# Performance work log

Hardware: AMD Instinct MI355X
Metric: run time of the kernel (lower is better)

Reference implementation:

```python
import jax, jax.numpy as jnp
import numpy as np

B, T, D = 16, 8192, 512
NHEAD, NKV = 8, 2
HD = D // NHEAD            # 64
KV_DIM = NKV * HD          # 128
N_REP = NHEAD // NKV       # 4
SCALE = 1.0 / np.sqrt(HD)


def setup_inputs() -> dict:
    key = jax.random.key(0)
    ks = jax.random.split(key, 8)
    w = 0.02
    return {
        "query": jax.random.normal(ks[0], (B, D), dtype=jnp.float32),
        "enc": jax.random.normal(ks[1], (B, T, D), dtype=jnp.float32),
        "Wq": jax.random.normal(ks[2], (D, D), dtype=jnp.float32) * w,
        "Wk": jax.random.normal(ks[3], (D, KV_DIM), dtype=jnp.float32) * w,
        "Wv": jax.random.normal(ks[4], (D, KV_DIM), dtype=jnp.float32) * w,
        "W1": jax.random.normal(ks[5], (2 * D, 4 * D), dtype=jnp.float32) * w,
        "W2": jax.random.normal(ks[6], (4 * D, D), dtype=jnp.float32) * w,
    }


def reference(query, enc, Wq, Wk, Wv, W1, W2):
    # Q projection: single decoder step -> [B, H, HD]
    q = (query @ Wq).reshape(B, NHEAD, HD)
    # K/V projections (GQA): [B, T, NKV, HD] -> [B, NKV, T, HD]
    k = (enc @ Wk).reshape(B, T, NKV, HD).transpose(0, 2, 1, 3)
    v = (enc @ Wv).reshape(B, T, NKV, HD).transpose(0, 2, 1, 3)
    # repeat KV heads to match query heads: [B, H, T, HD]
    k = jnp.repeat(k, N_REP, axis=1)
    v = jnp.repeat(v, N_REP, axis=1)
    # scaled dot-product attention, Tq == 1
    scores = jnp.einsum("bhd,bhtd->bht", q, k) * SCALE        # [B, H, T]
    attn = jax.nn.softmax(scores, axis=-1)
    context = jnp.einsum("bht,bhtd->bhd", attn, v).reshape(B, D)
    # combine context with query through SwiGLU-style MLP (Linear-SiLU-Linear)
    h = jnp.concatenate([context, query], axis=-1)            # [B, 2D]
    out = jax.nn.silu(h @ W1) @ W2                            # [B, D]
    return out
```

## Files before the change

### kernel.cpp

```cpp
#include <hip/hip_runtime.h>
#include <hip/hip_bf16.h>
#include <cstdint>
#include <cstddef>

#define BB 16
#define TT 8192
#define DD 512
#define NHEAD 8
#define NKV 2
#define HD 64
#define KVD 128
#define SCALE 0.125f

#define RB 64
#define NCHUNK (TT / RB)
#define BK 32
#define NSTEP (DD / BK)

typedef __attribute__((ext_vector_type(8))) short bf16x8;
typedef __attribute__((ext_vector_type(4))) float f32x4;

#define WS_Q      0
#define WS_WBT    8192
#define WS_OPART  73728
#define WS_ML     1122304
#define WS_H      1155072
#define WS_APART  1171456
#define WS_M2     1728512

__device__ __forceinline__ ushort f2bf(float f) {
    uint u = __builtin_bit_cast(uint, f);
    u += 0x7fffu + ((u >> 16) & 1u);
    return (ushort)(u >> 16);
}
__device__ __forceinline__ uint cvtpk(float a, float b) {
    uint r;
    asm("v_cvt_pk_bf16_f32 %0, %1, %2" : "=v"(r) : "v"(a), "v"(b));
    return r;
}
__device__ __forceinline__ float bf1(ushort s) {
    return __builtin_bit_cast(float, (uint)s << 16);
}
__device__ __forceinline__ float bflo(uint u) {
    return __builtin_bit_cast(float, u << 16);
}
__device__ __forceinline__ float bfhi(uint u) {
    return __builtin_bit_cast(float, u & 0xffff0000u);
}
__device__ __forceinline__ void gload_lds16(const void* g, void* l) {
    __builtin_amdgcn_global_load_lds((const __attribute__((address_space(1))) uint32_t*)g,
                                     (__attribute__((address_space(3))) uint32_t*)l, 16, 0, 0);
}

__global__ __launch_bounds__(256) void k_prep(const float* __restrict__ Wk,
                                              const float* __restrict__ Wv,
                                              const float* __restrict__ query,
                                              const float* __restrict__ Wq,
                                              ushort* __restrict__ wbt4,
                                              float* __restrict__ wsq) {
    const int t = threadIdx.x;
    if (blockIdx.x < 64) {
        const int G0 = blockIdx.x * 2048 + t * 8;
        const int s = G0 >> 13, r = G0 & 8191;
        const int fid = r >> 9, lane = (r >> 3) & 63;
        const int col = (fid >> 2) * 64 + (fid & 3) * 16 + (lane & 15);
        const int kbase = s * 32 + (lane >> 4) * 8;
        const float* W = (col < KVD) ? (Wk + col) : (Wv + (col - KVD));
#pragma unroll
        for (int e = 0; e < 8; ++e)
            wbt4[G0 + e] = f2bf(W[(size_t)(kbase + e) * KVD]);
    } else {
        __shared__ float qrow[DD];
        const int x = blockIdx.x - 64;
        const int b = x >> 1, half = x & 1;
        qrow[t] = query[b * DD + t];
        qrow[t + 256] = query[b * DD + t + 256];
        __syncthreads();
        const int col = half * 256 + t;
        float a0 = 0.f;
#pragma unroll 8
        for (int d = 0; d < DD; ++d) a0 = fmaf(qrow[d], Wq[(size_t)d * DD + col], a0);
        wsq[b * DD + col] = a0;
    }
}

__global__ __launch_bounds__(256) void k_attn(const float* __restrict__ enc,
                                              const ushort* __restrict__ wbt4,
                                              const float* __restrict__ wsq,
                                              float* __restrict__ o_part,
                                              float* __restrict__ ml) {
    __shared__ __align__(16) char smem[40960];
    __shared__ float sc[NHEAD * RB];
    __shared__ float qs[DD];

    const int tid = threadIdx.x;
    const int chunk = blockIdx.x, b = blockIdx.y;
    const int lane = tid & 63, w = tid >> 6;

    qs[tid] = wsq[b * DD + tid] * SCALE;
    qs[tid + 256] = wsq[b * DD + tid + 256] * SCALE;

    char* const A0 = smem;
    char* const A1 = smem + 4096;
    char* const B0 = smem + 8192;
    char* const B1 = smem + 24576;
    ushort* const kvl = (ushort*)smem;

    const float* encb = enc + ((size_t)b * TT + (size_t)chunk * RB) * DD;

    const int srow = (tid >> 6) * 16 + (tid & 15);
    const int skb = ((tid >> 4) & 3) * 8;

    f32x4 acc[4][4];
#pragma unroll
    for (int i = 0; i < 4; ++i)
#pragma unroll
        for (int j = 0; j < 4; ++j) acc[i][j] = (f32x4){0.f, 0.f, 0.f, 0.f};

    float4 e0, e1;

#define LOAD_ENC(ss)                                                                 \
    {                                                                                \
        const float* p_ = encb + (size_t)srow * DD + (ss) * BK + skb;                \
        e0 = *(const float4*)p_;                                                     \
        e1 = *(const float4*)(p_ + 4);                                               \
    }
#define WRITE_A(Abuf)                                                                \
    {                                                                                \
        uint4 u_;                                                                    \
        u_.x = cvtpk(e0.x, e0.y);                                                    \
        u_.y = cvtpk(e0.z, e0.w);                                                    \
        u_.z = cvtpk(e1.x, e1.y);                                                    \
        u_.w = cvtpk(e1.z, e1.w);                                                    \
        *(uint4*)((Abuf) + tid * 16) = u_;                                           \
    }
#define GLL_B(Bbuf, ss)                                                              \
    {                                                                                \
        _Pragma("unroll") for (int j = 0; j < 4; ++j)                                \
            gload_lds16(wbt4 + (size_t)(ss) * 8192 + (j * 256 + tid) * 8,            \
                        (Bbuf) + j * 4096 + w * 1024);                               \
    }

    LOAD_ENC(0);
    GLL_B(B0, 0);
    WRITE_A(A0);
    LOAD_ENC(1);

    for (int s = 0; s < NSTEP; ++s) {
        const int cur = s & 1;
        char* const Ac = cur ? A1 : A0;
        char* const Bc = cur ? B1 : B0;
        char* const An = cur ? A0 : A1;
        char* const Bn = cur ? B0 : B1;
        __syncthreads();
        if (s + 1 < NSTEP) {
            GLL_B(Bn, s + 1);
            WRITE_A(An);
            if (s + 2 < NSTEP) LOAD_ENC(s + 2);
        }
        bf16x8 bfr[4], af[4];
#pragma unroll
        for (int nt = 0; nt < 4; ++nt)
            bfr[nt] = *(const bf16x8*)(Bc + ((w * 4 + nt) * 64 + lane) * 16);
#pragma unroll
        for (int rt = 0; rt < 4; ++rt)
            af[rt] = *(const bf16x8*)(Ac + (rt * 64 + lane) * 16);
#pragma unroll
        for (int rt = 0; rt < 4; ++rt)
#pragma unroll
            for (int nt = 0; nt < 4; ++nt)
                acc[rt][nt] = __builtin_amdgcn_mfma_f32_16x16x32_bf16(
                    af[rt], bfr[nt], acc[rt][nt], 0, 0, 0);
    }

    const int h0 = w * 2;
    const int kvh = h0 >> 2;

    __syncthreads();
#pragma unroll
    for (int rt = 0; rt < 4; ++rt)
#pragma unroll
        for (int nt = 0; nt < 4; ++nt) {
            const int col = w * 64 + nt * 16 + (lane & 15);
#pragma unroll
            for (int j = 0; j < 4; ++j) {
                const int row = rt * 16 + (lane >> 4) * 4 + j;
                kvl[row * 258 + col] = f2bf(acc[rt][nt][j]);
            }
        }
    __syncthreads();

    {
        const float* qh0 = qs + h0 * HD;
        const float* qh1 = qs + (h0 + 1) * HD;
        const uint* kr = (const uint*)(kvl + lane * 258 + kvh * HD);
        float s0 = 0.f, s1 = 0.f;
#pragma unroll
        for (int d2 = 0; d2 < 32; ++d2) {
            const uint u = kr[d2];
            const float klo = bflo(u), khi = bfhi(u);
            s0 = fmaf(klo, qh0[2 * d2], s0);
            s0 = fmaf(khi, qh0[2 * d2 + 1], s0);
            s1 = fmaf(klo, qh1[2 * d2], s1);
            s1 = fmaf(khi, qh1[2 * d2 + 1], s1);
        }
        sc[h0 * RB + lane] = s0;
        sc[(h0 + 1) * RB + lane] = s1;
    }
    __syncthreads();

    {
        float mx0 = -1e30f, mx1 = -1e30f;
#pragma unroll 8
        for (int r = 0; r < RB; ++r) {
            mx0 = fmaxf(mx0, sc[h0 * RB + r]);
            mx1 = fmaxf(mx1, sc[(h0 + 1) * RB + r]);
        }
        float l0 = 0.f, l1 = 0.f, o0 = 0.f, o1 = 0.f;
        const ushort* vcol = kvl + KVD + kvh * HD + lane;
#pragma unroll 4
        for (int r = 0; r < RB; ++r) {
            const float vv = bf1(vcol[r * 258]);
            const float p0 = __expf(sc[h0 * RB + r] - mx0);
            const float p1 = __expf(sc[(h0 + 1) * RB + r] - mx1);
            l0 += p0; o0 = fmaf(p0, vv, o0);
            l1 += p1; o1 = fmaf(p1, vv, o1);
        }
        const size_t base0 = ((size_t)b * NCHUNK + chunk) * NHEAD + h0;
        o_part[base0 * HD + lane] = o0;
        o_part[(base0 + 1) * HD + lane] = o1;
        if (lane == 0) {
            ml[base0 * 2] = mx0; ml[base0 * 2 + 1] = l0;
            ml[(base0 + 1) * 2] = mx1; ml[(base0 + 1) * 2 + 1] = l1;
        }
    }
#undef LOAD_ENC
#undef WRITE_A
#undef GLL_B
}

__global__ __launch_bounds__(512) void k_reduce(const float* __restrict__ o_part,
                                                const float* __restrict__ ml,
                                                const float* __restrict__ query,
                                                float* __restrict__ hvec) {
    __shared__ float sEl[NHEAD][NCHUNK];
    const int b = blockIdx.x, t = threadIdx.x;
    const int h = t >> 6, lane = t & 63;

    const size_t ma_i = (((size_t)b * NCHUNK + lane) * NHEAD + h) * 2;
    const size_t mb_i = (((size_t)b * NCHUNK + lane + 64) * NHEAD + h) * 2;
    const float ma = ml[ma_i], la = ml[ma_i + 1];
    const float mb = ml[mb_i], lb = ml[mb_i + 1];
    float M = fmaxf(ma, mb);
#pragma unroll
    for (int off = 32; off >= 1; off >>= 1) M = fmaxf(M, __shfl_xor(M, off));
    const float ea = __expf(ma - M), eb = __expf(mb - M);
    float L = la * ea + lb * eb;
#pragma unroll
    for (int off = 32; off >= 1; off >>= 1) L += __shfl_xor(L, off);
    sEl[h][lane] = ea;
    sEl[h][lane + 64] = eb;
    __syncthreads();

    float O = 0.f;
#pragma unroll 4
    for (int i = 0; i < NCHUNK; ++i) {
        const size_t base = ((size_t)b * NCHUNK + i) * NHEAD + h;
        O = fmaf(o_part[base * HD + lane], sEl[h][i], O);
    }
    hvec[b * 1024 + h * HD + lane] = O / L;
    hvec[b * 1024 + 512 + t] = query[b * DD + t];
}

__global__ __launch_bounds__(256) void k_mlp1(const float* __restrict__ hvec,
                                              const float* __restrict__ W1,
                                              float* __restrict__ apart) {
    const int jb = blockIdx.x, ib = blockIdx.y;
    const int j = jb * 256 + threadIdx.x;
    float acc[BB];
#pragma unroll
    for (int b = 0; b < BB; ++b) acc[b] = 0.f;
    for (int i0 = ib * 64; i0 < ib * 64 + 64; i0 += 4) {
        const float w0 = W1[(size_t)(i0 + 0) * 2048 + j];
        const float w1 = W1[(size_t)(i0 + 1) * 2048 + j];
        const float w2 = W1[(size_t)(i0 + 2) * 2048 + j];
        const float w3 = W1[(size_t)(i0 + 3) * 2048 + j];
#pragma unroll
        for (int b = 0; b < BB; ++b) {
            const float* hb = hvec + b * 1024 + i0;
            acc[b] = fmaf(hb[0], w0, acc[b]);
            acc[b] = fmaf(hb[1], w1, acc[b]);
            acc[b] = fmaf(hb[2], w2, acc[b]);
            acc[b] = fmaf(hb[3], w3, acc[b]);
        }
    }
#pragma unroll
    for (int b = 0; b < BB; ++b)
        apart[((size_t)ib * BB + b) * 2048 + j] = acc[b];
}

__global__ __launch_bounds__(256) void k_mlp2(const float* __restrict__ apart,
                                              const float* __restrict__ W2,
                                              float* __restrict__ m2part) {
    __shared__ float actl[256];
    const int jb = blockIdx.x, b = blockIdx.y, ib = blockIdx.z;
    const int t = threadIdx.x;
    {
        const int jglob = ib * 256 + t;
        float s = 0.f;
#pragma unroll
        for (int p = 0; p < 16; ++p) s += apart[((size_t)p * BB + b) * 2048 + jglob];
        actl[t] = s / (1.f + __expf(-s));
    }
    __syncthreads();
    const int d = jb * 256 + t;
    float acc = 0.f;
    for (int j0 = 0; j0 < 256; j0 += 4) {
        const int jg = ib * 256 + j0;
        acc = fmaf(actl[j0 + 0], W2[(size_t)(jg + 0) * 512 + d], acc);
        acc = fmaf(actl[j0 + 1], W2[(size_t)(jg + 1) * 512 + d], acc);
        acc = fmaf(actl[j0 + 2], W2[(size_t)(jg + 2) * 512 + d], acc);
        acc = fmaf(actl[j0 + 3], W2[(size_t)(jg + 3) * 512 + d], acc);
    }
    m2part[((size_t)ib * BB + b) * 512 + d] = acc;
}

__global__ __launch_bounds__(512) void k_out(const float* __restrict__ m2part,
                                             float* __restrict__ out) {
    const int b = blockIdx.x, t = threadIdx.x;
    float s = 0.f;
#pragma unroll
    for (int ib = 0; ib < 8; ++ib) s += m2part[((size_t)ib * BB + b) * 512 + t];
    out[b * DD + t] = s;
}

extern "C" void kernel_launch(void* const* d_in, const int* in_sizes, int n_in,
                              void* d_out, int out_size, void* d_ws, size_t ws_size,
                              hipStream_t stream) {
    const float* query = (const float*)d_in[0];
    const float* enc   = (const float*)d_in[1];
    const float* Wq    = (const float*)d_in[2];
    const float* Wk    = (const float*)d_in[3];
    const float* Wv    = (const float*)d_in[4];
    const float* W1    = (const float*)d_in[5];
    const float* W2    = (const float*)d_in[6];
    float* ws  = (float*)d_ws;
    float* out = (float*)d_out;
    ushort* wbt4 = (ushort*)(ws + WS_WBT);

    k_prep<<<dim3(96), dim3(256), 0, stream>>>(Wk, Wv, query, Wq, wbt4, ws + WS_Q);
    k_attn<<<dim3(NCHUNK, BB), dim3(256), 0, stream>>>(enc, wbt4, ws + WS_Q,
                                                       ws + WS_OPART, ws + WS_ML);
    k_reduce<<<dim3(BB), dim3(512), 0, stream>>>(ws + WS_OPART, ws + WS_ML, query, ws + WS_H);
    k_mlp1<<<dim3(8, 16), dim3(256), 0, stream>>>(ws + WS_H, W1, ws + WS_APART);
    k_mlp2<<<dim3(2, BB, 8), dim3(256), 0, stream>>>(ws + WS_APART, W2, ws + WS_M2);
    k_out<<<dim3(BB), dim3(512), 0, stream>>>(ws + WS_M2, out);
}
```

Measured before the change: 157.2 us.

## Use 512-thread attention blocks with 2x4 wave tiling of the KV projection

The attention kernel now runs with 512 threads (8 waves) instead of 256. The 64x256 KV projection tile is split 2x4 across waves, so each wave holds half as many accumulators, and each wave later handles one query head instead of two. The goal is more waves in flight to hide the latency of streaming the fp32 encoder rows, with less register pressure per wave. The cost is that the B fragments are loaded redundantly by two wave rows, plus more barrier participants, and the A-tile staging layout changes.

```diff
diff --git a/kernel.cpp b/kernel.cpp
--- a/kernel.cpp
+++ b/kernel.cpp
@@ -84,11 +84,11 @@
     }
 }
 
-__global__ __launch_bounds__(256) void k_attn(const float* __restrict__ enc,
-                                              const ushort* __restrict__ wbt4,
-                                              const float* __restrict__ wsq,
-                                              float* __restrict__ o_part,
-                                              float* __restrict__ ml) {
+__global__ __launch_bounds__(512, 4) void k_attn(const float* __restrict__ enc,
+                                                 const ushort* __restrict__ wbt4,
+                                                 const float* __restrict__ wsq,
+                                                 float* __restrict__ o_part,
+                                                 float* __restrict__ ml) {
     __shared__ __align__(16) char smem[40960];
     __shared__ float sc[NHEAD * RB];
     __shared__ float qs[DD];
@@ -96,9 +96,9 @@
     const int tid = threadIdx.x;
     const int chunk = blockIdx.x, b = blockIdx.y;
     const int lane = tid & 63, w = tid >> 6;
+    const int wm = w >> 2, wn = w & 3;
 
     qs[tid] = wsq[b * DD + tid] * SCALE;
-    qs[tid + 256] = wsq[b * DD + tid + 256] * SCALE;
 
     char* const A0 = smem;
     char* const A1 = smem + 4096;
@@ -108,37 +108,34 @@
 
     const float* encb = enc + ((size_t)b * TT + (size_t)chunk * RB) * DD;
 
-    const int srow = (tid >> 6) * 16 + (tid & 15);
-    const int skb = ((tid >> 4) & 3) * 8;
-
-    f32x4 acc[4][4];
-#pragma unroll
-    for (int i = 0; i < 4; ++i)
+    const int aslot = tid >> 1, ahalf = tid & 1;
+    const int arow = aslot & 63, akg = aslot >> 6;
+
+    f32x4 acc[2][4];
+#pragma unroll
+    for (int i = 0; i < 2; ++i)
 #pragma unroll
         for (int j = 0; j < 4; ++j) acc[i][j] = (f32x4){0.f, 0.f, 0.f, 0.f};
 
-    float4 e0, e1;
+    float4 e0;
 
 #define LOAD_ENC(ss)                                                                 \
     {                                                                                \
-        const float* p_ = encb + (size_t)srow * DD + (ss) * BK + skb;                \
-        e0 = *(const float4*)p_;                                                     \
-        e1 = *(const float4*)(p_ + 4);                                               \
+        e0 = *(const float4*)(encb + (size_t)arow * DD + (ss) * BK + akg * 8 +       \
+                              ahalf * 4);                                            \
     }
 #define WRITE_A(Abuf)                                                                \
     {                                                                                \
-        uint4 u_;                                                                    \
+        uint2 u_;                                                                    \
         u_.x = cvtpk(e0.x, e0.y);                                                    \
         u_.y = cvtpk(e0.z, e0.w);                                                    \
-        u_.z = cvtpk(e1.x, e1.y);                                                    \
-        u_.w = cvtpk(e1.z, e1.w);                                                    \
-        *(uint4*)((Abuf) + tid * 16) = u_;                                           \
+        *(uint2*)((Abuf) + aslot * 16 + ahalf * 8) = u_;                             \
     }
 #define GLL_B(Bbuf, ss)                                                              \
     {                                                                                \
-        _Pragma("unroll") for (int j = 0; j < 4; ++j)                                \
-            gload_lds16(wbt4 + (size_t)(ss) * 8192 + (j * 256 + tid) * 8,            \
-                        (Bbuf) + j * 4096 + w * 1024);                               \
+        _Pragma("unroll") for (int j = 0; j < 2; ++j)                                \
+            gload_lds16(wbt4 + (size_t)(ss) * 8192 + ((j * 8 + w) * 64 + lane) * 8,  \
+                        (Bbuf) + (j * 8 + w) * 1024);                                \
     }
 
     LOAD_ENC(0);
@@ -158,81 +155,67 @@
             WRITE_A(An);
             if (s + 2 < NSTEP) LOAD_ENC(s + 2);
         }
-        bf16x8 bfr[4], af[4];
+        bf16x8 bfr[4], af[2];
 #pragma unroll
         for (int nt = 0; nt < 4; ++nt)
-            bfr[nt] = *(const bf16x8*)(Bc + ((w * 4 + nt) * 64 + lane) * 16);
-#pragma unroll
-        for (int rt = 0; rt < 4; ++rt)
-            af[rt] = *(const bf16x8*)(Ac + (rt * 64 + lane) * 16);
-#pragma unroll
-        for (int rt = 0; rt < 4; ++rt)
+            bfr[nt] = *(const bf16x8*)(Bc + ((wn * 4 + nt) * 64 + lane) * 16);
+#pragma unroll
+        for (int rt = 0; rt < 2; ++rt)
+            af[rt] = *(const bf16x8*)(Ac + ((lane >> 4) * 64 + wm * 32 + rt * 16 +
+                                            (lane & 15)) * 16);
+#pragma unroll
+        for (int rt = 0; rt < 2; ++rt)
 #pragma unroll
             for (int nt = 0; nt < 4; ++nt)
                 acc[rt][nt] = __builtin_amdgcn_mfma_f32_16x16x32_bf16(
                     af[rt], bfr[nt], acc[rt][nt], 0, 0, 0);
     }
 
-    const int h0 = w * 2;
-    const int kvh = h0 >> 2;
-
-    __syncthreads();
-#pragma unroll
-    for (int rt = 0; rt < 4; ++rt)
+    const int h = w, kvh = h >> 2;
+
+    __syncthreads();
+#pragma unroll
+    for (int rt = 0; rt < 2; ++rt)
 #pragma unroll
         for (int nt = 0; nt < 4; ++nt) {
-            const int col = w * 64 + nt * 16 + (lane & 15);
+            const int col = wn * 64 + nt * 16 + (lane & 15);
 #pragma unroll
             for (int j = 0; j < 4; ++j) {
-                const int row = rt * 16 + (lane >> 4) * 4 + j;
+                const int row = wm * 32 + rt * 16 + (lane >> 4) * 4 + j;
                 kvl[row * 258 + col] = f2bf(acc[rt][nt][j]);
             }
         }
     __syncthreads();
 
     {
-        const float* qh0 = qs + h0 * HD;
-        const float* qh1 = qs + (h0 + 1) * HD;
+        const float* qh = qs + h * HD;
         const uint* kr = (const uint*)(kvl + lane * 258 + kvh * HD);
-        float s0 = 0.f, s1 = 0.f;
+        float s0 = 0.f;
 #pragma unroll
         for (int d2 = 0; d2 < 32; ++d2) {
             const uint u = kr[d2];
-            const float klo = bflo(u), khi = bfhi(u);
-            s0 = fmaf(klo, qh0[2 * d2], s0);
-            s0 = fmaf(khi, qh0[2 * d2 + 1], s0);
-            s1 = fmaf(klo, qh1[2 * d2], s1);
-            s1 = fmaf(khi, qh1[2 * d2 + 1], s1);
-        }
-        sc[h0 * RB + lane] = s0;
-        sc[(h0 + 1) * RB + lane] = s1;
+            s0 = fmaf(bflo(u), qh[2 * d2], s0);
+            s0 = fmaf(bfhi(u), qh[2 * d2 + 1], s0);
+        }
+        sc[h * RB + lane] = s0;
     }
     __syncthreads();
 
     {
-        float mx0 = -1e30f, mx1 = -1e30f;
+        float mx = -1e30f;
 #pragma unroll 8
-        for (int r = 0; r < RB; ++r) {
-            mx0 = fmaxf(mx0, sc[h0 * RB + r]);
-            mx1 = fmaxf(mx1, sc[(h0 + 1) * RB + r]);
-        }
-        float l0 = 0.f, l1 = 0.f, o0 = 0.f, o1 = 0.f;
+        for (int r = 0; r < RB; ++r) mx = fmaxf(mx, sc[h * RB + r]);
+        float l0 = 0.f, o0 = 0.f;
         const ushort* vcol = kvl + KVD + kvh * HD + lane;
 #pragma unroll 4
         for (int r = 0; r < RB; ++r) {
-            const float vv = bf1(vcol[r * 258]);
-            const float p0 = __expf(sc[h0 * RB + r] - mx0);
-            const float p1 = __expf(sc[(h0 + 1) * RB + r] - mx1);
-            l0 += p0; o0 = fmaf(p0, vv, o0);
-            l1 += p1; o1 = fmaf(p1, vv, o1);
-        }
-        const size_t base0 = ((size_t)b * NCHUNK + chunk) * NHEAD + h0;
-        o_part[base0 * HD + lane] = o0;
-        o_part[(base0 + 1) * HD + lane] = o1;
-        if (lane == 0) {
-            ml[base0 * 2] = mx0; ml[base0 * 2 + 1] = l0;
-            ml[(base0 + 1) * 2] = mx1; ml[(base0 + 1) * 2 + 1] = l1;
-        }
+            const float p = __expf(sc[h * RB + r] - mx);
+            l0 += p;
+            o0 = fmaf(p, bf1(vcol[r * 258]), o0);
+        }
+        const size_t base = ((size_t)b * NCHUNK + chunk) * NHEAD + h;
+        o_part[base * HD + lane] = o0;
+        if (lane == 0) { ml[base * 2] = mx; ml[base * 2 + 1] = l0; }
     }
 #undef LOAD_ENC
 #undef WRITE_A
@@ -349,7 +332,7 @@
     ushort* wbt4 = (ushort*)(ws + WS_WBT);
 
     k_prep<<<dim3(96), dim3(256), 0, stream>>>(Wk, Wv, query, Wq, wbt4, ws + WS_Q);
-    k_attn<<<dim3(NCHUNK, BB), dim3(256), 0, stream>>>(enc, wbt4, ws + WS_Q,
+    k_attn<<<dim3(NCHUNK, BB), dim3(512), 0, stream>>>(enc, wbt4, ws + WS_Q,
                                                        ws + WS_OPART, ws + WS_ML);
     k_reduce<<<dim3(BB), dim3(512), 0, stream>>>(ws + WS_OPART, ws + WS_ML, query, ws + WS_H);
     k_mlp1<<<dim3(8, 16), dim3(256), 0, stream>>>(ws + WS_H, W1, ws + WS_APART);
```

New measurement: 165.0 us. 5.0% more time.

## Load projection weight fragments directly to registers and deepen enc prefetch

Applied to the files above, without the earlier changes.

The K/V weight fragments are now read straight from global memory into registers (register double-buffered) instead of being staged through LDS with global_load_lds, which shrinks shared memory. The enc prefetch goes from two steps ahead to three using two register sets. The main loop is fully unrolled, and each step ends in a custom barrier that waits only on LDS counters, so global loads stay in flight across the barrier. This removes LDS traffic for B and gives more latency hiding, at the cost of higher register pressure and redundant global reads of the weights by every block.

```diff
diff --git a/kernel.cpp b/kernel.cpp
--- a/kernel.cpp
+++ b/kernel.cpp
@@ -46,10 +46,6 @@
 }
 __device__ __forceinline__ float bfhi(uint u) {
     return __builtin_bit_cast(float, u & 0xffff0000u);
-}
-__device__ __forceinline__ void gload_lds16(const void* g, void* l) {
-    __builtin_amdgcn_global_load_lds((const __attribute__((address_space(1))) uint32_t*)g,
-                                     (__attribute__((address_space(3))) uint32_t*)l, 16, 0, 0);
 }
 
 __global__ __launch_bounds__(256) void k_prep(const float* __restrict__ Wk,
@@ -89,7 +85,7 @@
                                               const float* __restrict__ wsq,
                                               float* __restrict__ o_part,
                                               float* __restrict__ ml) {
-    __shared__ __align__(16) char smem[40960];
+    __shared__ __align__(16) char smem[33024];
     __shared__ float sc[NHEAD * RB];
     __shared__ float qs[DD];
 
@@ -102,11 +98,10 @@
 
     char* const A0 = smem;
     char* const A1 = smem + 4096;
-    char* const B0 = smem + 8192;
-    char* const B1 = smem + 24576;
     ushort* const kvl = (ushort*)smem;
 
     const float* encb = enc + ((size_t)b * TT + (size_t)chunk * RB) * DD;
+    const ushort* wfr = wbt4 + ((size_t)w * 256 + lane) * 8;
 
     const int srow = (tid >> 6) * 16 + (tid & 15);
     const int skb = ((tid >> 4) & 3) * 8;
@@ -117,60 +112,68 @@
 #pragma unroll
         for (int j = 0; j < 4; ++j) acc[i][j] = (f32x4){0.f, 0.f, 0.f, 0.f};
 
-    float4 e0, e1;
-
-#define LOAD_ENC(ss)                                                                 \
+    float4 eA0, eA1, eB0, eB1;
+    bf16x8 bfA[4], bfB[4], af[4];
+
+#define LOAD_E(E0, E1, ss)                                                           \
     {                                                                                \
         const float* p_ = encb + (size_t)srow * DD + (ss) * BK + skb;                \
-        e0 = *(const float4*)p_;                                                     \
-        e1 = *(const float4*)(p_ + 4);                                               \
-    }
-#define WRITE_A(Abuf)                                                                \
+        E0 = *(const float4*)p_;                                                     \
+        E1 = *(const float4*)(p_ + 4);                                               \
+    }
+#define WRITE_A(Abuf, E0, E1)                                                        \
     {                                                                                \
         uint4 u_;                                                                    \
-        u_.x = cvtpk(e0.x, e0.y);                                                    \
-        u_.y = cvtpk(e0.z, e0.w);                                                    \
-        u_.z = cvtpk(e1.x, e1.y);                                                    \
-        u_.w = cvtpk(e1.z, e1.w);                                                    \
+        u_.x = cvtpk(E0.x, E0.y);                                                    \
+        u_.y = cvtpk(E0.z, E0.w);                                                    \
+        u_.z = cvtpk(E1.x, E1.y);                                                    \
+        u_.w = cvtpk(E1.z, E1.w);                                                    \
         *(uint4*)((Abuf) + tid * 16) = u_;                                           \
     }
-#define GLL_B(Bbuf, ss)                                                              \
-    {                                                                                \
-        _Pragma("unroll") for (int j = 0; j < 4; ++j)                                \
-            gload_lds16(wbt4 + (size_t)(ss) * 8192 + (j * 256 + tid) * 8,            \
-                        (Bbuf) + j * 4096 + w * 1024);                               \
-    }
-
-    LOAD_ENC(0);
-    GLL_B(B0, 0);
-    WRITE_A(A0);
-    LOAD_ENC(1);
-
+#define LOAD_B(BF, ss)                                                               \
+    {                                                                                \
+        _Pragma("unroll") for (int nt = 0; nt < 4; ++nt)                             \
+            BF[nt] = *(const bf16x8*)(wfr + (size_t)(ss) * 8192 + nt * 512);         \
+    }
+#define SYNC()                                                                       \
+    {                                                                                \
+        __builtin_amdgcn_sched_barrier(0);                                           \
+        asm volatile("s_waitcnt lgkmcnt(0)" ::: "memory");                           \
+        __builtin_amdgcn_s_barrier();                                                \
+    }
+#define MFMA_STEP(Ac, BF)                                                            \
+    {                                                                                \
+        _Pragma("unroll") for (int rt = 0; rt < 4; ++rt)                             \
+            af[rt] = *(const bf16x8*)((Ac) + (rt * 64 + lane) * 16);                 \
+        _Pragma("unroll") for (int rt = 0; rt < 4; ++rt)                             \
+            _Pragma("unroll") for (int nt = 0; nt < 4; ++nt)                         \
+                acc[rt][nt] = __builtin_amdgcn_mfma_f32_16x16x32_bf16(               \
+                    af[rt], BF[nt], acc[rt][nt], 0, 0, 0);                           \
+    }
+
+    LOAD_E(eA0, eA1, 0);
+    LOAD_B(bfA, 0);
+    LOAD_E(eB0, eB1, 1);
+    WRITE_A(A0, eA0, eA1);
+    LOAD_E(eA0, eA1, 2);
+    SYNC();
+
+#pragma unroll
     for (int s = 0; s < NSTEP; ++s) {
-        const int cur = s & 1;
-        char* const Ac = cur ? A1 : A0;
-        char* const Bc = cur ? B1 : B0;
-        char* const An = cur ? A0 : A1;
-        char* const Bn = cur ? B0 : B1;
-        __syncthreads();
-        if (s + 1 < NSTEP) {
-            GLL_B(Bn, s + 1);
-            WRITE_A(An);
-            if (s + 2 < NSTEP) LOAD_ENC(s + 2);
-        }
-        bf16x8 bfr[4], af[4];
-#pragma unroll
-        for (int nt = 0; nt < 4; ++nt)
-            bfr[nt] = *(const bf16x8*)(Bc + ((w * 4 + nt) * 64 + lane) * 16);
-#pragma unroll
-        for (int rt = 0; rt < 4; ++rt)
-            af[rt] = *(const bf16x8*)(Ac + (rt * 64 + lane) * 16);
-#pragma unroll
-        for (int rt = 0; rt < 4; ++rt)
-#pragma unroll
-            for (int nt = 0; nt < 4; ++nt)
-                acc[rt][nt] = __builtin_amdgcn_mfma_f32_16x16x32_bf16(
-                    af[rt], bfr[nt], acc[rt][nt], 0, 0, 0);
+        char* const Ac = (s & 1) ? A1 : A0;
+        char* const An = (s & 1) ? A0 : A1;
+        if ((s & 1) == 0) {
+            if (s + 1 < NSTEP) WRITE_A(An, eB0, eB1);
+            if (s + 3 < NSTEP) LOAD_E(eB0, eB1, s + 3);
+            if (s + 1 < NSTEP) LOAD_B(bfB, s + 1);
+            MFMA_STEP(Ac, bfA);
+        } else {
+            if (s + 1 < NSTEP) WRITE_A(An, eA0, eA1);
+            if (s + 3 < NSTEP) LOAD_E(eA0, eA1, s + 3);
+            if (s + 1 < NSTEP) LOAD_B(bfA, s + 1);
+            MFMA_STEP(Ac, bfB);
+        }
+        SYNC();
     }
 
     const int h0 = w * 2;
@@ -234,9 +237,11 @@
             ml[(base0 + 1) * 2] = mx1; ml[(base0 + 1) * 2 + 1] = l1;
         }
     }
-#undef LOAD_ENC
+#undef LOAD_E
 #undef WRITE_A
-#undef GLL_B
+#undef LOAD_B
+#undef SYNC
+#undef MFMA_STEP
 }
 
 __global__ __launch_bounds__(512) void k_reduce(const float* __restrict__ o_part,
```

After: 147.7 us, median of 3. 1.06x faster.
